# Performance work log

Measured on AMD Instinct MI355X. Metric: run time of the kernel, lower is better.

Reference implementation:

```python
import jax, jax.numpy as jnp
import numpy as np

N_NODES = 50000
NEG_SLOPE = 0.2


def gat_conv(x, src, dst, W, al, ar, b):
    """DGL-style GATConv. x:[N,Fin] W:[Fin,H*D] al,ar:[H,D] b:[H*D] -> [N,H,D]."""
    H, D = al.shape
    feat = (x @ W).reshape(-1, H, D)                      # [N,H,D]
    el = jnp.sum(feat * al, axis=-1)                      # [N,H]
    er = jnp.sum(feat * ar, axis=-1)                      # [N,H]
    e = jax.nn.leaky_relu(el[src] + er[dst], NEG_SLOPE)   # [E,H] per-edge scores
    # segment softmax over incoming edges of each dst node
    m = jax.ops.segment_max(e, dst, num_segments=N_NODES)  # [N,H] (-inf for empty)
    ex = jnp.exp(e - m[dst])                              # [E,H]
    s = jax.ops.segment_sum(ex, dst, num_segments=N_NODES)  # [N,H]
    alpha = ex / s[dst]                                   # [E,H]
    msg = alpha[:, :, None] * feat[src]                   # [E,H,D]
    out = jax.ops.segment_sum(msg, dst, num_segments=N_NODES)  # [N,H,D]
    return out + b.reshape(1, H, D)


def setup_inputs() -> dict:
    key = jax.random.key(0)
    ks = jax.random.split(key, 12)
    E = 800000
    inp = {
        "x": jax.random.normal(ks[0], (N_NODES, 128), jnp.float32),
        "W1": jax.random.normal(ks[1], (2, 128, 128), jnp.float32) * 0.1,
        "al1": jax.random.normal(ks[2], (2, 4, 32), jnp.float32) * 0.1,
        "ar1": jax.random.normal(ks[3], (2, 4, 32), jnp.float32) * 0.1,
        "b1": jnp.zeros((2, 128), jnp.float32),
        "W2": jax.random.normal(ks[4], (2, 128, 64), jnp.float32) * 0.1,
        "al2": jax.random.normal(ks[5], (2, 1, 64), jnp.float32) * 0.1,
        "ar2": jax.random.normal(ks[6], (2, 1, 64), jnp.float32) * 0.1,
        "b2": jnp.zeros((2, 64), jnp.float32),
        "src": jax.random.randint(ks[7], (2, E), 0, N_NODES, jnp.int32),
        "dst": jax.random.randint(ks[8], (2, E), 0, N_NODES, jnp.int32),
    }
    return inp


def reference(x, W1, al1, ar1, b1, W2, al2, ar2, b2, src, dst):
    R = src.shape[0]  # number of meta-path relations
    # layer 1: HeteroGraphConv(sum over relations) -> elu(flatten heads)
    h1 = sum(gat_conv(x, src[r], dst[r], W1[r], al1[r], ar1[r], b1[r])
             for r in range(R))                           # [N,4,32]
    h1 = jax.nn.elu(h1.reshape(N_NODES, -1))              # [N,128]
    # layer 2: single head, mean over head dim
    h2 = sum(gat_conv(h1, src[r], dst[r], W2[r], al2[r], ar2[r], b2[r])
             for r in range(R))                           # [N,1,64]
    return jnp.mean(h2, axis=1)                           # [N,64]
```

## Files before the change

kernel.cpp:

```cpp
#include <hip/hip_runtime.h>
#include <hip/hip_bf16.h>
#include <math.h>

using bf16x8 = __attribute__((ext_vector_type(8))) short;
using f32x4  = __attribute__((ext_vector_type(4))) float;
using v4i    = __attribute__((ext_vector_type(4))) int;

#define NCH 32

__device__ __forceinline__ float b2f(unsigned short u) {
    return __uint_as_float(((unsigned)u) << 16);
}
__device__ __forceinline__ unsigned short f2b(float f) {
    unsigned u = __float_as_uint(f);
    return (unsigned short)((u + 0x7fff + ((u >> 16) & 1)) >> 16);
}

__global__ void k_prep(const float* __restrict__ x, unsigned short* __restrict__ xb, int n8,
                       const float* __restrict__ W1, const float* __restrict__ W2,
                       unsigned short* __restrict__ wt1, unsigned short* __restrict__ wt2,
                       unsigned* __restrict__ cnt, int ncnt, int nbx, int nbw) {
    int bid = blockIdx.x;
    if (bid < nbx) {
        int i = bid * 256 + threadIdx.x;
        if (i >= n8) return;
        float4 a = ((const float4*)x)[i * 2], b = ((const float4*)x)[i * 2 + 1];
        uint4 o;
        o.x = f2b(a.x) | ((unsigned)f2b(a.y) << 16);
        o.y = f2b(a.z) | ((unsigned)f2b(a.w) << 16);
        o.z = f2b(b.x) | ((unsigned)f2b(b.y) << 16);
        o.w = f2b(b.z) | ((unsigned)f2b(b.w) << 16);
        ((uint4*)xb)[i] = o;
    } else if (bid < nbx + nbw) {
        int i = (bid - nbx) * 256 + threadIdx.x;
        if (i < 32768) {
            int r = i >> 14, c = (i >> 7) & 127, k = i & 127;
            wt1[i] = f2b(W1[(r << 14) + (k << 7) + c]);
        } else {
            int j = i - 32768;
            if (j >= 16384) return;
            int r = j >> 13, c = (j >> 7) & 63, k = j & 127;
            wt2[j] = f2b(W2[r * 8192 + k * 64 + c]);
        }
    } else {
        int i = (bid - nbx - nbw) * 256 + threadIdx.x;
        if (i < ncnt) cnt[i] = 0u;
    }
}

__global__ void k_histp(const int* __restrict__ dst, unsigned* __restrict__ cnt, int E, int N) {
    const int part = blockIdx.x & 7, chunk = blockIdx.x >> 3;
    const int r = blockIdx.y;
    const int lo = part * (N / 8), hi = lo + N / 8;
    const int per = E / NCH;
    const int e0 = chunk * per, e1 = e0 + per;
    const int* dr = dst + (size_t)r * E;
    unsigned* cr = cnt + (size_t)r * N;
    for (int e = e0 + (int)threadIdx.x * 4; e < e1; e += 1024) {
        v4i d4 = *(const v4i*)(dr + e);
        if (d4.x >= lo && d4.x < hi) atomicAdd(&cr[d4.x], 1u);
        if (d4.y >= lo && d4.y < hi) atomicAdd(&cr[d4.y], 1u);
        if (d4.z >= lo && d4.z < hi) atomicAdd(&cr[d4.z], 1u);
        if (d4.w >= lo && d4.w < hi) atomicAdd(&cr[d4.w], 1u);
    }
}

#define SCAN_B 1024
__global__ void k_scanA(const unsigned* __restrict__ cnt, unsigned* __restrict__ bsum,
                        int n, int nb) {
    int r = blockIdx.y, b = blockIdx.x;
    int i0 = b * SCAN_B;
    unsigned s = 0;
    for (int t = threadIdx.x; t < SCAN_B; t += 256) {
        int i = i0 + t;
        if (i < n) s += cnt[(size_t)r * n + i];
    }
    __shared__ unsigned red[256];
    red[threadIdx.x] = s; __syncthreads();
    for (int st = 128; st > 0; st >>= 1) {
        if ((int)threadIdx.x < st) red[threadIdx.x] += red[threadIdx.x + st];
        __syncthreads();
    }
    if (threadIdx.x == 0) bsum[r * nb + b] = red[0];
}
__global__ void k_scanB(unsigned* __restrict__ bsum, unsigned* __restrict__ off, int n, int nb) {
    int r = threadIdx.x >> 6, l = threadIdx.x & 63;
    if (r >= 2) return;
    unsigned orig = (l < nb) ? bsum[r * nb + l] : 0u;
    unsigned v = orig;
    for (int st = 1; st < 64; st <<= 1) {
        unsigned t = __shfl_up(v, st);
        if (l >= st) v += t;
    }
    unsigned total = __shfl(v, 63);
    if (l < nb) bsum[r * nb + l] = v - orig;
    if (l == 0) off[(size_t)r * (n + 1) + n] = total;
}
__global__ void k_scanC(unsigned* __restrict__ cnt, const unsigned* __restrict__ bsum,
                        unsigned* __restrict__ off, int n, int nb) {
    int r = blockIdx.y, b = blockIdx.x;
    int i0 = b * SCAN_B + (int)threadIdx.x * 4;
    unsigned v[4]; unsigned s = 0;
#pragma unroll
    for (int j = 0; j < 4; j++) {
        int i = i0 + j;
        v[j] = (i < n) ? cnt[(size_t)r * n + i] : 0u;
        s += v[j];
    }
    __shared__ unsigned red[256];
    red[threadIdx.x] = s; __syncthreads();
    for (int st = 1; st < 256; st <<= 1) {
        unsigned t = ((int)threadIdx.x >= st) ? red[threadIdx.x - st] : 0u;
        __syncthreads();
        red[threadIdx.x] += t;
        __syncthreads();
    }
    unsigned run = bsum[r * nb + b] + red[threadIdx.x] - s;
#pragma unroll
    for (int j = 0; j < 4; j++) {
        int i = i0 + j;
        if (i < n) {
            off[(size_t)r * (n + 1) + i] = run;
            cnt[(size_t)r * n + i] = run;
        }
        run += v[j];
    }
}

__device__ __forceinline__ void scat_body(int bid, const int* __restrict__ src,
                                          const int* __restrict__ dst, unsigned* __restrict__ cur,
                                          unsigned short* __restrict__ csr, int E, int N) {
    const int part = bid & 7;
    const int q = bid >> 3;
    const int r = q & 1, chunk = q >> 1;
    const int lo = part * (N / 8), hi = lo + N / 8;
    const int per = E / NCH;
    const int e0 = chunk * per, e1 = e0 + per;
    const int* dr = dst + (size_t)r * E;
    const int* sr = src + (size_t)r * E;
    unsigned* curr = cur + (size_t)r * N;
    unsigned short* csrr = csr + (size_t)r * E;
    for (int e = e0 + (int)threadIdx.x * 4; e < e1; e += 1024) {
        v4i d4 = *(const v4i*)(dr + e);
        bool m0 = (d4.x >= lo) & (d4.x < hi);
        bool m1 = (d4.y >= lo) & (d4.y < hi);
        bool m2 = (d4.z >= lo) & (d4.z < hi);
        bool m3 = (d4.w >= lo) & (d4.w < hi);
        if (m0 | m1 | m2 | m3) {
            v4i s4 = *(const v4i*)(sr + e);
            if (m0) { unsigned p = atomicAdd(&curr[d4.x], 1u); csrr[p] = (unsigned short)s4.x; }
            if (m1) { unsigned p = atomicAdd(&curr[d4.y], 1u); csrr[p] = (unsigned short)s4.y; }
            if (m2) { unsigned p = atomicAdd(&curr[d4.z], 1u); csrr[p] = (unsigned short)s4.z; }
            if (m3) { unsigned p = atomicAdd(&curr[d4.w], 1u); csrr[p] = (unsigned short)s4.w; }
        }
    }
}

template <int M, int H>
__device__ __forceinline__ void gemm_body(int xblk, int r,
        const unsigned short* __restrict__ Xb, const unsigned short* __restrict__ Wt0,
        const float* __restrict__ alv, const float* __restrict__ arv,
        unsigned short* __restrict__ feat0, float* __restrict__ el, float* __restrict__ er,
        int N, unsigned short* xs, unsigned short* ws) {
    constexpr int D = M / H;
    const unsigned short* Wt = Wt0 + (size_t)r * M * 128;
    unsigned short* outp = feat0 + (size_t)r * N * M;
    float* elr = el + (size_t)r * N * H;
    float* err = er + (size_t)r * N * H;
    const int tid = threadIdx.x;
    const int row0 = xblk * 64;
    for (int ch = tid; ch < 64 * 16; ch += 256) {
        int rr = ch >> 4, c16 = ch & 15;
        int gr = row0 + rr;
        uint4 v = make_uint4(0, 0, 0, 0);
        if (gr < N) v = ((const uint4*)(Xb + (size_t)gr * 128))[c16];
        int byte = rr * 256 + ((c16 * 16) ^ ((rr & 7) << 4));
        *(uint4*)((char*)xs + byte) = v;
    }
    for (int ch = tid; ch < M * 16; ch += 256) {
        int rr = ch >> 4, c16 = ch & 15;
        uint4 v = ((const uint4*)(Wt + (size_t)rr * 128))[c16];
        int byte = rr * 256 + ((c16 * 16) ^ ((rr & 7) << 4));
        *(uint4*)((char*)ws + byte) = v;
    }
    __syncthreads();
    const int w = tid >> 6, l = tid & 63;
    const int sub = l & 15;
    const int ar_ = w * 16 + sub;
    const int kg = l >> 4;
    bf16x8 a[4];
#pragma unroll
    for (int k4 = 0; k4 < 4; k4++) {
        int byte = ar_ * 256 + (((kg * 16) + k4 * 64) ^ ((ar_ & 7) << 4));
        a[k4] = *(const bf16x8*)((const char*)xs + byte);
    }
    float alr[M / 16], arr[M / 16];
#pragma unroll
    for (int ct = 0; ct < M / 16; ct++) {
        alr[ct] = alv[(size_t)r * M + ct * 16 + sub];
        arr[ct] = arv[(size_t)r * M + ct * 16 + sub];
    }
    float pel[H][4], per[H][4];
#pragma unroll
    for (int h = 0; h < H; h++)
#pragma unroll
        for (int q = 0; q < 4; q++) { pel[h][q] = 0.f; per[h][q] = 0.f; }

#pragma unroll
    for (int ct = 0; ct < M / 16; ct++) {
        f32x4 acc = {0.f, 0.f, 0.f, 0.f};
        const int bc = ct * 16 + sub;
#pragma unroll
        for (int k4 = 0; k4 < 4; k4++) {
            int byte = bc * 256 + (((kg * 16) + k4 * 64) ^ ((bc & 7) << 4));
            bf16x8 bfr = *(const bf16x8*)((const char*)ws + byte);
            acc = __builtin_amdgcn_mfma_f32_16x16x32_bf16(a[k4], bfr, acc, 0, 0, 0);
        }
        const int hct = (ct * 16) / D;
#pragma unroll
        for (int q = 0; q < 4; q++) {
            pel[hct][q] += acc[q] * alr[ct];
            per[hct][q] += acc[q] * arr[ct];
        }
#pragma unroll
        for (int q = 0; q < 4; q++) {
            int gr = row0 + w * 16 + kg * 4 + q;
            if (gr < N) outp[(size_t)gr * M + ct * 16 + sub] = f2b(acc[q]);
        }
    }
#pragma unroll
    for (int h = 0; h < H; h++)
#pragma unroll
        for (int q = 0; q < 4; q++) {
            float v = pel[h][q], u = per[h][q];
#pragma unroll
            for (int o = 8; o > 0; o >>= 1) { v += __shfl_xor(v, o); u += __shfl_xor(u, o); }
            pel[h][q] = v; per[h][q] = u;
        }
#pragma unroll
    for (int h = 0; h < H; h++) {
        if (sub == h) {
#pragma unroll
            for (int q = 0; q < 4; q++) {
                int gr = row0 + w * 16 + kg * 4 + q;
                if (gr < N) { elr[(size_t)gr * H + h] = pel[h][q]; err[(size_t)gr * H + h] = per[h][q]; }
            }
        }
    }
}

__global__ __launch_bounds__(256) void k_scatgemm(
    const int* __restrict__ src, const int* __restrict__ dst,
    unsigned* __restrict__ cur, unsigned short* __restrict__ csr, int E, int N, int scatBlocks,
    const unsigned short* __restrict__ Xb, const unsigned short* __restrict__ Wt0,
    const float* __restrict__ alv, const float* __restrict__ arv,
    unsigned short* __restrict__ feat0, float* __restrict__ el, float* __restrict__ er) {
    __shared__ __align__(16) unsigned short xs[64 * 128];
    __shared__ __align__(16) unsigned short ws[128 * 128];
    int bid = blockIdx.x;
    if (bid < scatBlocks) {
        scat_body(bid, src, dst, cur, csr, E, N);
    } else {
        int g = bid - scatBlocks;
        gemm_body<128, 4>(g >> 1, g & 1, Xb, Wt0, alv, arv, feat0, el, er, N, xs, ws);
    }
}

__global__ __launch_bounds__(256) void k_gemm2(
    const unsigned short* __restrict__ Xb, const unsigned short* __restrict__ Wt0,
    const float* __restrict__ alv, const float* __restrict__ arv,
    unsigned short* __restrict__ feat0, float* __restrict__ el, float* __restrict__ er, int N) {
    __shared__ __align__(16) unsigned short xs[64 * 128];
    __shared__ __align__(16) unsigned short ws[64 * 128];
    gemm_body<64, 1>(blockIdx.x, blockIdx.y, Xb, Wt0, alv, arv, feat0, el, er, N, xs, ws);
}

template <int ELUF>
__global__ __launch_bounds__(256) void k_node_gat1(
    const unsigned* __restrict__ off, const unsigned short* __restrict__ csr_src,
    const float* __restrict__ el, const float* __restrict__ er,
    const unsigned short* __restrict__ feat0, const unsigned short* __restrict__ feat1,
    const float* __restrict__ bias, unsigned* __restrict__ outp, int N, int E) {
    constexpr int H = 4, HD = 128;
    __shared__ float s_w[4][4 * 64];
    __shared__ int s_sid[4][64];
    const int wslot = threadIdx.x >> 6;
    const int lane = threadIdx.x & 63;
    const int n = (blockIdx.x * 256 + threadIdx.x) >> 6;
    if (n >= N) return;
    const int c0 = lane * 2;
    const int h = c0 / 32;
    const unsigned laneoff = (unsigned)lane << 2;

    float res[2] = {0.f, 0.f};

    for (int r = 0; r < 2; r++) {
        const char* __restrict__ featc = (const char*)(r ? feat1 : feat0);
        const float* elr = el + (size_t)r * N * H;
        const float* ernp = er + (size_t)r * N * H + (size_t)n * H;
        float ern[H];
#pragma unroll
        for (int hh = 0; hh < H; hh++) ern[hh] = ernp[hh];
        const unsigned* offr = off + (size_t)r * (N + 1);
        const unsigned short* srcs = csr_src + (size_t)r * E;
        const unsigned o0 = offr[n], o1 = offr[n + 1];

        float den = 0.f;
        float acc[2] = {0.f, 0.f};

        for (unsigned base = o0; base < o1; base += 64) {
            const int cnt = (int)min(64u, o1 - base);
            if (lane < cnt) {
                unsigned sv = srcs[base + lane];
                s_sid[wslot][lane] = (int)sv;
                float4 e4 = *(const float4*)(elr + (size_t)sv * 4);
                float v0 = e4.x + ern[0]; v0 = v0 > 0.f ? v0 : 0.2f * v0;
                float v1 = e4.y + ern[1]; v1 = v1 > 0.f ? v1 : 0.2f * v1;
                float v2 = e4.z + ern[2]; v2 = v2 > 0.f ? v2 : 0.2f * v2;
                float v3 = e4.w + ern[3]; v3 = v3 > 0.f ? v3 : 0.2f * v3;
                float4 wv = make_float4(__expf(v0), __expf(v1), __expf(v2), __expf(v3));
                *(float4*)&s_w[wslot][lane * 4] = wv;
            }
            asm volatile("s_waitcnt lgkmcnt(0)" ::: "memory");
#pragma unroll 8
            for (int j = 0; j < cnt; j++) {
                unsigned sv = (unsigned)s_sid[wslot][j];
                float wv = s_w[wslot][j * 4 + h];
                den += wv;
                unsigned u = *(const unsigned*)(featc + ((sv << 8) + laneoff));
                acc[0] += wv * __uint_as_float(u << 16);
                acc[1] += wv * __uint_as_float(u & 0xffff0000u);
            }
        }
        if (den > 0.f) {
            float inv = 1.f / den;
            res[0] += acc[0] * inv;
            res[1] += acc[1] * inv;
        }
    }
    float v0 = res[0] + bias[c0] + bias[HD + c0];
    float v1 = res[1] + bias[c0 + 1] + bias[HD + c0 + 1];
    if (ELUF) { v0 = v0 > 0.f ? v0 : expm1f(v0); v1 = v1 > 0.f ? v1 : expm1f(v1); }
    outp[((size_t)n * HD + c0) / 2] = f2b(v0) | ((unsigned)f2b(v1) << 16);
}

__global__ __launch_bounds__(256) void k_node_gat2(
    const unsigned* __restrict__ off, const unsigned short* __restrict__ csr_src,
    const float* __restrict__ el, const float* __restrict__ er,
    const unsigned short* __restrict__ feat0, const unsigned short* __restrict__ feat1,
    const float* __restrict__ bias, float* __restrict__ outp, int N, int E) {
    __shared__ uint2 s_ws[4][64];
    const int wslot = threadIdx.x >> 6;
    const int lane = threadIdx.x & 63;
    const int n = (blockIdx.x * 256 + threadIdx.x) >> 6;
    if (n >= N) return;
    const int sub = lane & 31, half = lane >> 5;
    const unsigned laneoff = (unsigned)sub << 2;

    float res[2] = {0.f, 0.f};

    for (int r = 0; r < 2; r++) {
        const char* __restrict__ featc = (const char*)(r ? feat1 : feat0);
        const float* elr = el + (size_t)r * N;
        const float ern = er[(size_t)r * N + n];
        const unsigned* offr = off + (size_t)r * (N + 1);
        const unsigned short* srcs = csr_src + (size_t)r * E;
        const unsigned o0 = offr[n], o1 = offr[n + 1];

        float den = 0.f;
        float acc[2] = {0.f, 0.f};

        for (unsigned base = o0; base < o1; base += 64) {
            const int cnt = (int)min(64u, o1 - base);
            if (lane < cnt) {
                unsigned sv = srcs[base + lane];
                float v = elr[sv] + ern; v = v > 0.f ? v : 0.2f * v;
                s_ws[wslot][lane] = make_uint2(sv, __float_as_uint(__expf(v)));
            }
            asm volatile("s_waitcnt lgkmcnt(0)" ::: "memory");
#pragma unroll 4
            for (int j2 = 0; j2 < cnt; j2 += 2) {
                int jj = j2 + half;
                int jjc = jj < cnt ? jj : 0;
                uint2 sw = s_ws[wslot][jjc];
                float wv = (jj < cnt) ? __uint_as_float(sw.y) : 0.f;
                den += wv;
                unsigned u = *(const unsigned*)(featc + (((size_t)sw.x << 7) + laneoff));
                acc[0] += wv * __uint_as_float(u << 16);
                acc[1] += wv * __uint_as_float(u & 0xffff0000u);
            }
        }
        acc[0] += __shfl_xor(acc[0], 32);
        acc[1] += __shfl_xor(acc[1], 32);
        den += __shfl_xor(den, 32);
        if (den > 0.f) {
            float inv = 1.f / den;
            res[0] += acc[0] * inv;
            res[1] += acc[1] * inv;
        }
    }
    if (half == 0) {
        int c = sub * 2;
        float v0 = res[0] + bias[c] + bias[64 + c];
        float v1 = res[1] + bias[c + 1] + bias[64 + c + 1];
        *(float2*)(outp + (size_t)n * 64 + c) = make_float2(v0, v1);
    }
}

extern "C" void kernel_launch(void* const* d_in, const int* in_sizes, int n_in,
                              void* d_out, int out_size, void* d_ws, size_t ws_size,
                              hipStream_t stream) {
    const float* x   = (const float*)d_in[0];
    const float* W1  = (const float*)d_in[1];
    const float* al1 = (const float*)d_in[2];
    const float* ar1 = (const float*)d_in[3];
    const float* b1  = (const float*)d_in[4];
    const float* W2  = (const float*)d_in[5];
    const float* al2 = (const float*)d_in[6];
    const float* ar2 = (const float*)d_in[7];
    const float* b2  = (const float*)d_in[8];
    const int* src   = (const int*)d_in[9];
    const int* dst   = (const int*)d_in[10];

    const int N = in_sizes[0] / 128;
    const int E = in_sizes[9] / 2;
    float* out = (float*)d_out;

    char* w = (char*)d_ws;
    unsigned short* xb   = (unsigned short*)w; w += (size_t)N * 128 * 2;
    unsigned short* feat = (unsigned short*)w; w += (size_t)2 * N * 128 * 2;
    unsigned short* h1b  = (unsigned short*)w; w += (size_t)N * 128 * 2;
    unsigned short* wt1  = (unsigned short*)w; w += (size_t)2 * 128 * 128 * 2;
    unsigned short* wt2  = (unsigned short*)w; w += (size_t)2 * 64 * 128 * 2;
    float* el      = (float*)w; w += (size_t)2 * N * 4 * 4;
    float* er      = (float*)w; w += (size_t)2 * N * 4 * 4;
    unsigned* cnt  = (unsigned*)w; w += (size_t)2 * N * 4;
    unsigned* off  = (unsigned*)w; w += (size_t)2 * (N + 1) * 4;
    unsigned* bsum = (unsigned*)w; w += 2 * 64 * 4;
    unsigned short* csr_src = (unsigned short*)w; w += (size_t)2 * E * 2;

    auto cdiv = [](long long a, long long b) { return (int)((a + b - 1) / b); };
    const int NB = cdiv(N, SCAN_B);

    const int nbx = cdiv((long long)N * 16, 256);
    const int nbw = cdiv(49152, 256);
    const int nbz = cdiv(2LL * N, 256);
    k_prep<<<nbx + nbw + nbz, 256, 0, stream>>>(x, xb, N * 16, W1, W2, wt1, wt2, cnt, 2 * N, nbx, nbw);

    { dim3 g(NCH * 8, 2); k_histp<<<g, 256, 0, stream>>>(dst, cnt, E, N); }
    { dim3 g(NB, 2); k_scanA<<<g, 256, 0, stream>>>(cnt, bsum, N, NB); }
    k_scanB<<<1, 128, 0, stream>>>(bsum, off, N, NB);
    { dim3 g(NB, 2); k_scanC<<<g, 256, 0, stream>>>(cnt, bsum, off, N, NB); }

    const int scatBlocks = NCH * 8 * 2;
    const int gemmBlocks = cdiv(N, 64) * 2;
    k_scatgemm<<<scatBlocks + gemmBlocks, 256, 0, stream>>>(
        src, dst, cnt, csr_src, E, N, scatBlocks, xb, wt1, al1, ar1, feat, el, er);

    k_node_gat1<1><<<cdiv(N, 4), 256, 0, stream>>>(off, csr_src, el, er,
        feat, feat + (size_t)N * 128, b1, (unsigned*)h1b, N, E);

    { dim3 g(cdiv(N, 64), 2);
      k_gemm2<<<g, 256, 0, stream>>>(h1b, wt2, al2, ar2, feat, el, er, N); }
    k_node_gat2<<<cdiv(N, 4), 256, 0, stream>>>(off, csr_src, el, er,
        feat, feat + (size_t)N * 64, b2, out, N, E);
}
```

Measured before the change: 286.4 us.

## Compress edge indices to 16-bit and split GAT1 gather across half-waves

A new prep stage packs the int32 src/dst arrays into 16-bit copies. The histogram and scatter passes, which each re-read the edge list eight times (once per node partition), now read half as many bytes. The layer-1 node aggregation now has each half-wave handle alternate edges with 8-byte feature loads, and the two halves are combined with a cross-lane shuffle. This adds one conversion pass and an extra workspace, and relies on node ids fitting in 16 bits.

```diff
diff --git a/kernel.cpp b/kernel.cpp
--- a/kernel.cpp
+++ b/kernel.cpp
@@ -19,7 +19,10 @@
 __global__ void k_prep(const float* __restrict__ x, unsigned short* __restrict__ xb, int n8,
                        const float* __restrict__ W1, const float* __restrict__ W2,
                        unsigned short* __restrict__ wt1, unsigned short* __restrict__ wt2,
-                       unsigned* __restrict__ cnt, int ncnt, int nbx, int nbw) {
+                       unsigned* __restrict__ cnt, int ncnt,
+                       const int* __restrict__ src, const int* __restrict__ dst,
+                       unsigned short* __restrict__ src16, unsigned short* __restrict__ dst16,
+                       int nE2, int nbx, int nbw, int nbz) {
     int bid = blockIdx.x;
     if (bid < nbx) {
         int i = bid * 256 + threadIdx.x;
@@ -42,26 +45,44 @@
             int r = j >> 13, c = (j >> 7) & 63, k = j & 127;
             wt2[j] = f2b(W2[r * 8192 + k * 64 + c]);
         }
-    } else {
+    } else if (bid < nbx + nbw + nbz) {
         int i = (bid - nbx - nbw) * 256 + threadIdx.x;
         if (i < ncnt) cnt[i] = 0u;
-    }
-}
-
-__global__ void k_histp(const int* __restrict__ dst, unsigned* __restrict__ cnt, int E, int N) {
+    } else {
+        int i = (bid - nbx - nbw - nbz) * 256 + threadIdx.x;
+        if (i >= nE2) return;
+        v4i sa = *(const v4i*)(src + i * 8), sb = *(const v4i*)(src + i * 8 + 4);
+        v4i da = *(const v4i*)(dst + i * 8), db = *(const v4i*)(dst + i * 8 + 4);
+        uint4 so, do_;
+        so.x = (unsigned)(sa.x & 0xffff) | ((unsigned)sa.y << 16);
+        so.y = (unsigned)(sa.z & 0xffff) | ((unsigned)sa.w << 16);
+        so.z = (unsigned)(sb.x & 0xffff) | ((unsigned)sb.y << 16);
+        so.w = (unsigned)(sb.z & 0xffff) | ((unsigned)sb.w << 16);
+        do_.x = (unsigned)(da.x & 0xffff) | ((unsigned)da.y << 16);
+        do_.y = (unsigned)(da.z & 0xffff) | ((unsigned)da.w << 16);
+        do_.z = (unsigned)(db.x & 0xffff) | ((unsigned)db.y << 16);
+        do_.w = (unsigned)(db.z & 0xffff) | ((unsigned)db.w << 16);
+        ((uint4*)src16)[i] = so;
+        ((uint4*)dst16)[i] = do_;
+    }
+}
+
+__global__ void k_histp(const unsigned short* __restrict__ dst16, unsigned* __restrict__ cnt,
+                        int E, int N) {
     const int part = blockIdx.x & 7, chunk = blockIdx.x >> 3;
     const int r = blockIdx.y;
     const int lo = part * (N / 8), hi = lo + N / 8;
     const int per = E / NCH;
     const int e0 = chunk * per, e1 = e0 + per;
-    const int* dr = dst + (size_t)r * E;
+    const unsigned short* dr = dst16 + (size_t)r * E;
     unsigned* cr = cnt + (size_t)r * N;
-    for (int e = e0 + (int)threadIdx.x * 4; e < e1; e += 1024) {
-        v4i d4 = *(const v4i*)(dr + e);
-        if (d4.x >= lo && d4.x < hi) atomicAdd(&cr[d4.x], 1u);
-        if (d4.y >= lo && d4.y < hi) atomicAdd(&cr[d4.y], 1u);
-        if (d4.z >= lo && d4.z < hi) atomicAdd(&cr[d4.z], 1u);
-        if (d4.w >= lo && d4.w < hi) atomicAdd(&cr[d4.w], 1u);
+    for (int e = e0 + (int)threadIdx.x * 8; e < e1; e += 2048) {
+        uint4 u = *(const uint4*)(dr + e);
+        int d[8] = {(int)(u.x & 0xffff), (int)(u.x >> 16), (int)(u.y & 0xffff), (int)(u.y >> 16),
+                    (int)(u.z & 0xffff), (int)(u.z >> 16), (int)(u.w & 0xffff), (int)(u.w >> 16)};
+#pragma unroll
+        for (int t = 0; t < 8; t++)
+            if (d[t] >= lo && d[t] < hi) atomicAdd(&cr[d[t]], 1u);
     }
 }
 
@@ -127,8 +148,9 @@
     }
 }
 
-__device__ __forceinline__ void scat_body(int bid, const int* __restrict__ src,
-                                          const int* __restrict__ dst, unsigned* __restrict__ cur,
+__device__ __forceinline__ void scat_body(int bid, const unsigned short* __restrict__ src16,
+                                          const unsigned short* __restrict__ dst16,
+                                          unsigned* __restrict__ cur,
                                           unsigned short* __restrict__ csr, int E, int N) {
     const int part = bid & 7;
     const int q = bid >> 3;
@@ -136,22 +158,30 @@
     const int lo = part * (N / 8), hi = lo + N / 8;
     const int per = E / NCH;
     const int e0 = chunk * per, e1 = e0 + per;
-    const int* dr = dst + (size_t)r * E;
-    const int* sr = src + (size_t)r * E;
+    const unsigned short* dr = dst16 + (size_t)r * E;
+    const unsigned short* sr = src16 + (size_t)r * E;
     unsigned* curr = cur + (size_t)r * N;
     unsigned short* csrr = csr + (size_t)r * E;
-    for (int e = e0 + (int)threadIdx.x * 4; e < e1; e += 1024) {
-        v4i d4 = *(const v4i*)(dr + e);
-        bool m0 = (d4.x >= lo) & (d4.x < hi);
-        bool m1 = (d4.y >= lo) & (d4.y < hi);
-        bool m2 = (d4.z >= lo) & (d4.z < hi);
-        bool m3 = (d4.w >= lo) & (d4.w < hi);
-        if (m0 | m1 | m2 | m3) {
-            v4i s4 = *(const v4i*)(sr + e);
-            if (m0) { unsigned p = atomicAdd(&curr[d4.x], 1u); csrr[p] = (unsigned short)s4.x; }
-            if (m1) { unsigned p = atomicAdd(&curr[d4.y], 1u); csrr[p] = (unsigned short)s4.y; }
-            if (m2) { unsigned p = atomicAdd(&curr[d4.z], 1u); csrr[p] = (unsigned short)s4.z; }
-            if (m3) { unsigned p = atomicAdd(&curr[d4.w], 1u); csrr[p] = (unsigned short)s4.w; }
+    for (int e = e0 + (int)threadIdx.x * 8; e < e1; e += 2048) {
+        uint4 u = *(const uint4*)(dr + e);
+        int d[8] = {(int)(u.x & 0xffff), (int)(u.x >> 16), (int)(u.y & 0xffff), (int)(u.y >> 16),
+                    (int)(u.z & 0xffff), (int)(u.z >> 16), (int)(u.w & 0xffff), (int)(u.w >> 16)};
+        bool any = false;
+#pragma unroll
+        for (int t = 0; t < 8; t++) any |= (d[t] >= lo && d[t] < hi);
+        if (any) {
+            uint4 su = *(const uint4*)(sr + e);
+            unsigned short s[8] = {(unsigned short)(su.x & 0xffff), (unsigned short)(su.x >> 16),
+                                   (unsigned short)(su.y & 0xffff), (unsigned short)(su.y >> 16),
+                                   (unsigned short)(su.z & 0xffff), (unsigned short)(su.z >> 16),
+                                   (unsigned short)(su.w & 0xffff), (unsigned short)(su.w >> 16)};
+#pragma unroll
+            for (int t = 0; t < 8; t++) {
+                if (d[t] >= lo && d[t] < hi) {
+                    unsigned p = atomicAdd(&curr[d[t]], 1u);
+                    csrr[p] = s[t];
+                }
+            }
         }
     }
 }
@@ -250,7 +280,7 @@
 }
 
 __global__ __launch_bounds__(256) void k_scatgemm(
-    const int* __restrict__ src, const int* __restrict__ dst,
+    const unsigned short* __restrict__ src16, const unsigned short* __restrict__ dst16,
     unsigned* __restrict__ cur, unsigned short* __restrict__ csr, int E, int N, int scatBlocks,
     const unsigned short* __restrict__ Xb, const unsigned short* __restrict__ Wt0,
     const float* __restrict__ alv, const float* __restrict__ arv,
@@ -259,7 +289,7 @@
     __shared__ __align__(16) unsigned short ws[128 * 128];
     int bid = blockIdx.x;
     if (bid < scatBlocks) {
-        scat_body(bid, src, dst, cur, csr, E, N);
+        scat_body(bid, src16, dst16, cur, csr, E, N);
     } else {
         int g = bid - scatBlocks;
         gemm_body<128, 4>(g >> 1, g & 1, Xb, Wt0, alv, arv, feat0, el, er, N, xs, ws);
@@ -282,17 +312,18 @@
     const unsigned short* __restrict__ feat0, const unsigned short* __restrict__ feat1,
     const float* __restrict__ bias, unsigned* __restrict__ outp, int N, int E) {
     constexpr int H = 4, HD = 128;
-    __shared__ float s_w[4][4 * 64];
+    __shared__ float s_w[4][64][4];
     __shared__ int s_sid[4][64];
     const int wslot = threadIdx.x >> 6;
     const int lane = threadIdx.x & 63;
     const int n = (blockIdx.x * 256 + threadIdx.x) >> 6;
     if (n >= N) return;
-    const int c0 = lane * 2;
-    const int h = c0 / 32;
-    const unsigned laneoff = (unsigned)lane << 2;
-
-    float res[2] = {0.f, 0.f};
+    const int sub = lane & 31, half = lane >> 5;
+    const int c0 = sub * 4;
+    const int h = sub >> 3;
+    const unsigned laneoff = (unsigned)sub << 3;
+
+    float res[4] = {0.f, 0.f, 0.f, 0.f};
 
     for (int r = 0; r < 2; r++) {
         const char* __restrict__ featc = (const char*)(r ? feat1 : feat0);
@@ -306,7 +337,7 @@
         const unsigned o0 = offr[n], o1 = offr[n + 1];
 
         float den = 0.f;
-        float acc[2] = {0.f, 0.f};
+        float acc[4] = {0.f, 0.f, 0.f, 0.f};
 
         for (unsigned base = o0; base < o1; base += 64) {
             const int cnt = (int)min(64u, o1 - base);
@@ -318,30 +349,48 @@
                 float v1 = e4.y + ern[1]; v1 = v1 > 0.f ? v1 : 0.2f * v1;
                 float v2 = e4.z + ern[2]; v2 = v2 > 0.f ? v2 : 0.2f * v2;
                 float v3 = e4.w + ern[3]; v3 = v3 > 0.f ? v3 : 0.2f * v3;
-                float4 wv = make_float4(__expf(v0), __expf(v1), __expf(v2), __expf(v3));
-                *(float4*)&s_w[wslot][lane * 4] = wv;
+                *(float4*)&s_w[wslot][lane][0] =
+                    make_float4(__expf(v0), __expf(v1), __expf(v2), __expf(v3));
             }
             asm volatile("s_waitcnt lgkmcnt(0)" ::: "memory");
-#pragma unroll 8
-            for (int j = 0; j < cnt; j++) {
-                unsigned sv = (unsigned)s_sid[wslot][j];
-                float wv = s_w[wslot][j * 4 + h];
+#pragma unroll 4
+            for (int j2 = 0; j2 < cnt; j2 += 2) {
+                const int jj = j2 + half;
+                const bool val = jj < cnt;
+                const int jjc = val ? jj : 0;
+                unsigned sv = (unsigned)s_sid[wslot][jjc];
+                float wv = val ? s_w[wslot][jjc][h] : 0.f;
                 den += wv;
-                unsigned u = *(const unsigned*)(featc + ((sv << 8) + laneoff));
-                acc[0] += wv * __uint_as_float(u << 16);
-                acc[1] += wv * __uint_as_float(u & 0xffff0000u);
+                uint2 u = *(const uint2*)(featc + ((sv << 8) + laneoff));
+                acc[0] += wv * __uint_as_float(u.x << 16);
+                acc[1] += wv * __uint_as_float(u.x & 0xffff0000u);
+                acc[2] += wv * __uint_as_float(u.y << 16);
+                acc[3] += wv * __uint_as_float(u.y & 0xffff0000u);
             }
         }
+#pragma unroll
+        for (int f = 0; f < 4; f++) acc[f] += __shfl_xor(acc[f], 32);
+        den += __shfl_xor(den, 32);
         if (den > 0.f) {
             float inv = 1.f / den;
-            res[0] += acc[0] * inv;
-            res[1] += acc[1] * inv;
-        }
-    }
-    float v0 = res[0] + bias[c0] + bias[HD + c0];
-    float v1 = res[1] + bias[c0 + 1] + bias[HD + c0 + 1];
-    if (ELUF) { v0 = v0 > 0.f ? v0 : expm1f(v0); v1 = v1 > 0.f ? v1 : expm1f(v1); }
-    outp[((size_t)n * HD + c0) / 2] = f2b(v0) | ((unsigned)f2b(v1) << 16);
+#pragma unroll
+            for (int f = 0; f < 4; f++) res[f] += acc[f] * inv;
+        }
+    }
+    if (half == 0) {
+        float v[4];
+#pragma unroll
+        for (int f = 0; f < 4; f++) {
+            int c = c0 + f;
+            float t = res[f] + bias[c] + bias[HD + c];
+            if (ELUF) t = t > 0.f ? t : expm1f(t);
+            v[f] = t;
+        }
+        uint2 o;
+        o.x = f2b(v[0]) | ((unsigned)f2b(v[1]) << 16);
+        o.y = f2b(v[2]) | ((unsigned)f2b(v[3]) << 16);
+        *(uint2*)&outp[((size_t)n * HD + c0) / 2] = o;
+    }
 }
 
 __global__ __launch_bounds__(256) void k_node_gat2(
@@ -427,17 +476,19 @@
     float* out = (float*)d_out;
 
     char* w = (char*)d_ws;
-    unsigned short* xb   = (unsigned short*)w; w += (size_t)N * 128 * 2;
-    unsigned short* feat = (unsigned short*)w; w += (size_t)2 * N * 128 * 2;
-    unsigned short* h1b  = (unsigned short*)w; w += (size_t)N * 128 * 2;
-    unsigned short* wt1  = (unsigned short*)w; w += (size_t)2 * 128 * 128 * 2;
-    unsigned short* wt2  = (unsigned short*)w; w += (size_t)2 * 64 * 128 * 2;
-    float* el      = (float*)w; w += (size_t)2 * N * 4 * 4;
-    float* er      = (float*)w; w += (size_t)2 * N * 4 * 4;
-    unsigned* cnt  = (unsigned*)w; w += (size_t)2 * N * 4;
-    unsigned* off  = (unsigned*)w; w += (size_t)2 * (N + 1) * 4;
-    unsigned* bsum = (unsigned*)w; w += 2 * 64 * 4;
+    unsigned short* xb    = (unsigned short*)w; w += (size_t)N * 128 * 2;
+    unsigned short* feat  = (unsigned short*)w; w += (size_t)2 * N * 128 * 2;
+    unsigned short* h1b   = (unsigned short*)w; w += (size_t)N * 128 * 2;
+    unsigned short* wt1   = (unsigned short*)w; w += (size_t)2 * 128 * 128 * 2;
+    unsigned short* wt2   = (unsigned short*)w; w += (size_t)2 * 64 * 128 * 2;
+    float* el       = (float*)w; w += (size_t)2 * N * 4 * 4;
+    float* er       = (float*)w; w += (size_t)2 * N * 4 * 4;
+    unsigned* cnt   = (unsigned*)w; w += (size_t)2 * N * 4;
+    unsigned* off   = (unsigned*)w; w += (size_t)2 * (N + 1) * 4;
+    unsigned* bsum  = (unsigned*)w; w += 2 * 64 * 4;
     unsigned short* csr_src = (unsigned short*)w; w += (size_t)2 * E * 2;
+    unsigned short* src16   = (unsigned short*)w; w += (size_t)2 * E * 2;
+    unsigned short* dst16   = (unsigned short*)w; w += (size_t)2 * E * 2;
 
     auto cdiv = [](long long a, long long b) { return (int)((a + b - 1) / b); };
     const int NB = cdiv(N, SCAN_B);
@@ -445,9 +496,12 @@
     const int nbx = cdiv((long long)N * 16, 256);
     const int nbw = cdiv(49152, 256);
     const int nbz = cdiv(2LL * N, 256);
-    k_prep<<<nbx + nbw + nbz, 256, 0, stream>>>(x, xb, N * 16, W1, W2, wt1, wt2, cnt, 2 * N, nbx, nbw);
-
-    { dim3 g(NCH * 8, 2); k_histp<<<g, 256, 0, stream>>>(dst, cnt, E, N); }
+    const int nE2 = 2 * E / 8;
+    const int nbe = cdiv(nE2, 256);
+    k_prep<<<nbx + nbw + nbz + nbe, 256, 0, stream>>>(
+        x, xb, N * 16, W1, W2, wt1, wt2, cnt, 2 * N, src, dst, src16, dst16, nE2, nbx, nbw, nbz);
+
+    { dim3 g(NCH * 8, 2); k_histp<<<g, 256, 0, stream>>>(dst16, cnt, E, N); }
     { dim3 g(NB, 2); k_scanA<<<g, 256, 0, stream>>>(cnt, bsum, N, NB); }
     k_scanB<<<1, 128, 0, stream>>>(bsum, off, N, NB);
     { dim3 g(NB, 2); k_scanC<<<g, 256, 0, stream>>>(cnt, bsum, off, N, NB); }
@@ -455,7 +509,7 @@
     const int scatBlocks = NCH * 8 * 2;
     const int gemmBlocks = cdiv(N, 64) * 2;
     k_scatgemm<<<scatBlocks + gemmBlocks, 256, 0, stream>>>(
-        src, dst, cnt, csr_src, E, N, scatBlocks, xb, wt1, al1, ar1, feat, el, er);
+        src16, dst16, cnt, csr_src, E, N, scatBlocks, xb, wt1, al1, ar1, feat, el, er);
 
     k_node_gat1<1><<<cdiv(N, 4), 256, 0, stream>>>(off, csr_src, el, er,
         feat, feat + (size_t)N * 128, b1, (unsigned*)h1b, N, E);
```

Result: slower. 295.6 us (+3.2%).
